# Kernel optimization log

Measured on AMD Instinct MI355X. Metric: run time of the kernel, lower is better.

Reference implementation:

```python
import jax, jax.numpy as jnp
import numpy as np

S, B, E, H = 2048, 2, 1024, 16
DH = E // H
SCALING = DH ** -0.5


def setup_inputs() -> dict:
    key = jax.random.key(0)
    ks = jax.random.split(key, 9)
    std = 1.0 / np.sqrt(E)
    return {
        "query": jax.random.normal(ks[0], (S, B, E), jnp.float32),
        "wq": jax.random.normal(ks[1], (E, E), jnp.float32) * std,
        "bq": jax.random.normal(ks[2], (E,), jnp.float32) * 0.02,
        "wk": jax.random.normal(ks[3], (E, E), jnp.float32) * std,
        "bk": jax.random.normal(ks[4], (E,), jnp.float32) * 0.02,
        "wv": jax.random.normal(ks[5], (E, E), jnp.float32) * std,
        "bv": jax.random.normal(ks[6], (E,), jnp.float32) * 0.02,
        "wo": jax.random.normal(ks[7], (E, E), jnp.float32) * std,
        "bo": jax.random.normal(ks[8], (E,), jnp.float32) * 0.02,
    }


def reference(query, wq, bq, wk, bk, wv, bv, wo, bo):
    # query: [S, B, E] (time, batch, channel), self-attention: key=value=query
    q = (query @ wq.T + bq) * SCALING          # fairseq scales q, not scores
    k = query @ wk.T + bk
    v = query @ wv.T + bv
    # split heads: [S, B, H, DH]
    q = q.reshape(S, B, H, DH)
    k = k.reshape(S, B, H, DH)
    v = v.reshape(S, B, H, DH)
    scores = jnp.einsum("qbhd,kbhd->bhqk", q, k)   # [B, H, S, S]
    probs = jax.nn.softmax(scores, axis=-1)
    ctx = jnp.einsum("bhqk,kbhd->qbhd", probs, v)  # [S, B, H, DH]
    ctx = ctx.reshape(S, B, E)
    return ctx @ wo.T + bo                          # [S, B, E]
```

## Files before the change

### kernel.cpp

```cpp
#include <hip/hip_runtime.h>
#include <hip/hip_bf16.h>
#include <stdint.h>

#define S_LEN 2048
#define BATCH 2
#define EMB   1024
#define NH    16
#define DHEAD 64
#define ROWS  (S_LEN*BATCH)
#define SCALE_Q 0.18033688011112042f
#define DEFER_THR 11.0f

typedef __attribute__((ext_vector_type(8))) short bf16x8;
typedef __attribute__((ext_vector_type(4))) float f32x4;
typedef __attribute__((ext_vector_type(16))) float f32x16;

typedef const __attribute__((address_space(1))) void* gas_ptr;
typedef __attribute__((address_space(3))) void* las_ptr;
#define GLD16(g, l) __builtin_amdgcn_global_load_lds((gas_ptr)(g), (las_ptr)(l), 16, 0, 0)

__device__ __forceinline__ unsigned short f2b(float f) {
  union { float f; unsigned int u; } v; v.f = f;
  unsigned int u = v.u;
  unsigned int r = (u + 0x7FFFu + ((u >> 16) & 1u)) >> 16;
  return (unsigned short)r;
}

__device__ __forceinline__ unsigned cvt_pk_bf16(float lo, float hi) {
  unsigned r;
  asm("v_cvt_pk_bf16_f32 %0, %1, %2" : "=v"(r) : "v"(lo), "v"(hi));
  return r;
}

__device__ __forceinline__ float exp2_raw(float x) {
  float r;
  asm("v_exp_f32 %0, %1" : "=v"(r) : "v"(x));
  return r;
}

__device__ __forceinline__ void cvt8(const float* __restrict__ s,
                                     unsigned short* __restrict__ d, size_t i) {
  float4 a = *reinterpret_cast<const float4*>(s + i);
  float4 b = *reinterpret_cast<const float4*>(s + i + 4);
  uint4 o;
  o.x = (unsigned)f2b(a.x) | ((unsigned)f2b(a.y) << 16);
  o.y = (unsigned)f2b(a.z) | ((unsigned)f2b(a.w) << 16);
  o.z = (unsigned)f2b(b.x) | ((unsigned)f2b(b.y) << 16);
  o.w = (unsigned)f2b(b.z) | ((unsigned)f2b(b.w) << 16);
  *reinterpret_cast<uint4*>(d + i) = o;
}

__global__ __launch_bounds__(256) void cvt_all_kernel(
    const float* __restrict__ query,
    const float* __restrict__ wq, const float* __restrict__ wk,
    const float* __restrict__ wv, const float* __restrict__ wo,
    unsigned short* __restrict__ Xbf,
    unsigned short* __restrict__ Wqb, unsigned short* __restrict__ Wkb,
    unsigned short* __restrict__ Wvb, unsigned short* __restrict__ Wob) {
  int id = blockIdx.x;
  const float* s; unsigned short* d; size_t off;
  if (id < 2048) { s = query; d = Xbf; off = (size_t)id * 2048; }
  else {
    int wsel = (id - 2048) >> 9;
    off = (size_t)((id - 2048) & 511) * 2048;
    switch (wsel) {
      case 0:  s = wq; d = Wqb; break;
      case 1:  s = wk; d = Wkb; break;
      case 2:  s = wv; d = Wvb; break;
      default: s = wo; d = Wob; break;
    }
  }
  cvt8(s, d, off + (size_t)threadIdx.x * 8);
}

__device__ __forceinline__ void gemm_mainloop(const unsigned short* __restrict__ A,
                                              const unsigned short* __restrict__ Bw,
                                              int m0, int n0, f32x4 acc[4][4],
                                              unsigned short* Ab, unsigned short* Bb) {
  const int t    = threadIdx.x;
  const int lane = t & 63;
  const int w    = t >> 6;
  const int wr   = w >> 1, wc = w & 1;
  const int lm   = lane & 15;
  const int lq   = lane >> 4;

  f32x4 zf = {0.0f, 0.0f, 0.0f, 0.0f};
#pragma unroll
  for (int i = 0; i < 4; ++i)
#pragma unroll
    for (int j = 0; j < 4; ++j) acc[i][j] = zf;

  for (int k0 = 0; k0 < EMB; k0 += 64) {
#pragma unroll
    for (int q = 0; q < 4; ++q) {
      int c = t + q * 256;
      int r = c >> 3, ci = c & 7;
      int lc = ci ^ (r & 7);
      GLD16(A  + (size_t)(m0 + r) * EMB + k0 + lc * 8,
            (char*)Ab + (size_t)(q * 256 + w * 64) * 16);
      GLD16(Bw + (size_t)(n0 + r) * EMB + k0 + lc * 8,
            (char*)Bb + (size_t)(q * 256 + w * 64) * 16);
    }
    asm volatile("s_waitcnt vmcnt(0)" ::: "memory");
    __syncthreads();

#pragma unroll
    for (int kk = 0; kk < 2; ++kk) {
      bf16x8 af[4], bfr[4];
#pragma unroll
      for (int i = 0; i < 4; ++i) {
        int ra = wr * 64 + i * 16 + lm;
        af[i] = *reinterpret_cast<const bf16x8*>(
            &Ab[ra * 64 + ((kk * 4 + lq) ^ (ra & 7)) * 8]);
      }
#pragma unroll
      for (int j = 0; j < 4; ++j) {
        int rb = wc * 64 + j * 16 + lm;
        bfr[j] = *reinterpret_cast<const bf16x8*>(
            &Bb[rb * 64 + ((kk * 4 + lq) ^ (rb & 7)) * 8]);
      }
#pragma unroll
      for (int i = 0; i < 4; ++i)
#pragma unroll
        for (int j = 0; j < 4; ++j)
          acc[i][j] = __builtin_amdgcn_mfma_f32_16x16x32_bf16(af[i], bfr[j], acc[i][j], 0, 0, 0);
    }
    __syncthreads();
  }
}

__global__ __launch_bounds__(256) void gemm_qkv_kernel(
    const unsigned short* __restrict__ X,
    const unsigned short* __restrict__ Wq, const unsigned short* __restrict__ Wk,
    const unsigned short* __restrict__ Wv,
    const float* __restrict__ bq, const float* __restrict__ bk, const float* __restrict__ bv,
    unsigned short* __restrict__ Qb, unsigned short* __restrict__ Kb,
    unsigned short* __restrict__ Vtg) {
  __shared__ unsigned short SH[2][128 * 64];
  const int m0 = blockIdx.x * 128;
  const int n0 = blockIdx.y * 128;
  const int z  = blockIdx.z;
  const unsigned short* Bw = (z == 0) ? Wq : (z == 1) ? Wk : Wv;
  const float* bias        = (z == 0) ? bq : (z == 1) ? bk : bv;

  f32x4 acc[4][4];
  gemm_mainloop(X, Bw, m0, n0, acc, SH[0], SH[1]);

  const int t    = threadIdx.x;
  const int lane = t & 63;
  const int w    = t >> 6;
  const int wr   = w >> 1, wc = w & 1;
  const int lm   = lane & 15, lq = lane >> 4;

  if (z != 2) {
    unsigned short* Out = (z == 0) ? Qb : Kb;
    const float scale   = (z == 0) ? SCALE_Q : 1.0f;
#pragma unroll
    for (int j = 0; j < 4; ++j) {
      int col = n0 + wc * 64 + j * 16 + lm;
      int h = col >> 6, dd = col & 63;
      float bc = bias[col];
#pragma unroll
      for (int i = 0; i < 4; ++i) {
#pragma unroll
        for (int r = 0; r < 4; ++r) {
          int row = m0 + wr * 64 + i * 16 + lq * 4 + r;
          int s = row >> 1, b = row & 1;
          float v = (acc[i][j][r] + bc) * scale;
          Out[((size_t)(b * NH + h) * S_LEN + s) * DHEAD + dd] = f2b(v);
        }
      }
    }
  } else {
    unsigned short* T = &SH[0][0];
#pragma unroll
    for (int j = 0; j < 4; ++j) {
      int col = wc * 64 + j * 16 + lm;
      float bc = bias[n0 + col];
#pragma unroll
      for (int i = 0; i < 4; ++i) {
#pragma unroll
        for (int r = 0; r < 4; ++r) {
          int row = wr * 64 + i * 16 + lq * 4 + r;
          int idx = (row & 1) * 64 + (row >> 1);
          int chunk = idx >> 3, within = idx & 7;
          int pchunk = (chunk & 8) | ((chunk ^ col) & 7);
          T[col * 128 + pchunk * 8 + within] = f2b(acc[i][j][r] + bc);
        }
      }
    }
    __syncthreads();
#pragma unroll
    for (int itr = 0; itr < 8; ++itr) {
      int u = (t >> 3) + itr * 32;
      int col = u & 127, b = u >> 7;
      int c3 = t & 7;
      int pchunk = (b * 8) | ((c3 ^ col) & 7);
      bf16x8 vv = *reinterpret_cast<const bf16x8*>(&T[col * 128 + pchunk * 8]);
      int h = (n0 + col) >> 6, dd = (n0 + col) & 63;
      unsigned short* dst =
          Vtg + ((size_t)(b * NH + h) * DHEAD + dd) * S_LEN + (m0 >> 1);
      int p1 = ((c3 >> 1) << 4) | ((c3 & 1) << 2);
      union { bf16x8 v; uint4 u4; } cv; cv.v = vv;
      *reinterpret_cast<uint2*>(dst + p1)     = make_uint2(cv.u4.x, cv.u4.y);
      *reinterpret_cast<uint2*>(dst + p1 + 8) = make_uint2(cv.u4.z, cv.u4.w);
    }
  }
}

__global__ __launch_bounds__(256) void gemm_out_kernel(
    const unsigned short* __restrict__ Ctx, const unsigned short* __restrict__ Wo,
    const float* __restrict__ bo, float* __restrict__ Out) {
  __shared__ unsigned short Ab[64 * 64];
  __shared__ unsigned short Bb[128 * 64];
  const int m0 = blockIdx.x * 64;
  const int n0 = blockIdx.y * 128;
  const int t    = threadIdx.x;
  const int lane = t & 63;
  const int w    = t >> 6;
  const int wr   = w >> 1, wc = w & 1;
  const int lm   = lane & 15, lq = lane >> 4;

  f32x4 zf = {0.0f, 0.0f, 0.0f, 0.0f};
  f32x4 acc[2][4];
#pragma unroll
  for (int i = 0; i < 2; ++i)
#pragma unroll
    for (int j = 0; j < 4; ++j) acc[i][j] = zf;

  for (int k0 = 0; k0 < EMB; k0 += 64) {
#pragma unroll
    for (int q = 0; q < 2; ++q) {
      int c = t + q * 256;
      int r = c >> 3, ci = c & 7;
      int lc = ci ^ (r & 7);
      GLD16(Ctx + (size_t)(m0 + r) * EMB + k0 + lc * 8,
            (char*)Ab + (size_t)(q * 256 + w * 64) * 16);
    }
#pragma unroll
    for (int q = 0; q < 4; ++q) {
      int c = t + q * 256;
      int r = c >> 3, ci = c & 7;
      int lc = ci ^ (r & 7);
      GLD16(Wo + (size_t)(n0 + r) * EMB + k0 + lc * 8,
            (char*)Bb + (size_t)(q * 256 + w * 64) * 16);
    }
    asm volatile("s_waitcnt vmcnt(0)" ::: "memory");
    __syncthreads();

#pragma unroll
    for (int kk = 0; kk < 2; ++kk) {
      bf16x8 af[2], bfr[4];
#pragma unroll
      for (int i = 0; i < 2; ++i) {
        int ra = wr * 32 + i * 16 + lm;
        af[i] = *reinterpret_cast<const bf16x8*>(
            &Ab[ra * 64 + ((kk * 4 + lq) ^ (ra & 7)) * 8]);
      }
#pragma unroll
      for (int j = 0; j < 4; ++j) {
        int rb = wc * 64 + j * 16 + lm;
        bfr[j] = *reinterpret_cast<const bf16x8*>(
            &Bb[rb * 64 + ((kk * 4 + lq) ^ (rb & 7)) * 8]);
      }
#pragma unroll
      for (int i = 0; i < 2; ++i)
#pragma unroll
        for (int j = 0; j < 4; ++j)
          acc[i][j] = __builtin_amdgcn_mfma_f32_16x16x32_bf16(af[i], bfr[j], acc[i][j], 0, 0, 0);
    }
    __syncthreads();
  }

#pragma unroll
  for (int j = 0; j < 4; ++j) {
    int col = n0 + wc * 64 + j * 16 + lm;
    float bc = bo[col];
#pragma unroll
    for (int i = 0; i < 2; ++i) {
#pragma unroll
      for (int r = 0; r < 4; ++r) {
        int row = m0 + wr * 32 + i * 16 + lq * 4 + r;
        Out[(size_t)row * EMB + col] = acc[i][j][r] + bc;
      }
    }
  }
}

__global__ __launch_bounds__(512, 4) void attn_kernel(
    const unsigned short* __restrict__ Qb, const unsigned short* __restrict__ Kb,
    const unsigned short* __restrict__ Vtg, unsigned short* __restrict__ Ctx) {
  const int bh = blockIdx.x;
  const int q0 = blockIdx.y * 128;
  const int t    = threadIdx.x;
  const int lane = t & 63;
  const int w    = t >> 6;
  const int hf   = w >> 2;
  const int wl   = w & 3;
  const int th   = t & 255;
  const int l31  = lane & 31;
  const int hh   = lane >> 5;
  const unsigned short* Q  = Qb  + (size_t)bh * S_LEN * DHEAD;
  const unsigned short* K  = Kb  + (size_t)bh * S_LEN * DHEAD;
  const unsigned short* Vt = Vtg + (size_t)bh * DHEAD * S_LEN;

  alignas(16) __shared__ char SMEM[65536];
  unsigned short* Kl = (unsigned short*)(SMEM + hf * 32768);
  unsigned short* Vl = (unsigned short*)(SMEM + hf * 32768 + 16384);

  const int qw = q0 + wl * 32;

  bf16x8 aq[4];
#pragma unroll
  for (int kk = 0; kk < 4; ++kk)
    aq[kk] = *reinterpret_cast<const bf16x8*>(
        Q + (size_t)(qw + l31) * DHEAD + kk * 16 + hh * 8);

  f32x16 z16 = {0.f,0.f,0.f,0.f, 0.f,0.f,0.f,0.f, 0.f,0.f,0.f,0.f, 0.f,0.f,0.f,0.f};
  f32x16 accO[2];
  accO[0] = z16; accO[1] = z16;
  float m_s = -1e30f, l_s = 0.0f;

  auto STAGE = [&](int b, int kb) {
#pragma unroll
    for (int q = 0; q < 2; ++q) {
      int c = th + q * 256;
      int r = c >> 3, pp = c & 7;
      int lc = pp ^ (r & 7);
      GLD16(K + (size_t)(kb + r) * DHEAD + lc * 8,
            (char*)Kl + (size_t)b * 8192 + (size_t)(q * 256 + wl * 64) * 16);
      GLD16(Vt + (size_t)r * S_LEN + kb + lc * 8,
            (char*)Vl + (size_t)b * 8192 + (size_t)(q * 256 + wl * 64) * 16);
    }
  };

  const int kvbase = hf * (S_LEN / 2);
  const int NT = S_LEN / 2 / 64;
  STAGE(0, kvbase);
  STAGE(1, kvbase + 64);

  for (int it = 0; it < NT; ++it) {
    const int cur = it & 1;
    if (it < NT - 1) {
      asm volatile("s_waitcnt vmcnt(4)" ::: "memory");
    } else {
      asm volatile("s_waitcnt vmcnt(0)" ::: "memory");
    }
    __builtin_amdgcn_s_barrier();

    const unsigned short* Klc = Kl + cur * 4096;
    const unsigned short* Vlc = Vl + cur * 4096;

    f32x16 p32[2];
    __builtin_amdgcn_s_setprio(1);
#pragma unroll
    for (int ji = 0; ji < 2; ++ji) {
      f32x16 a = z16;
      int rr = ji * 32 + l31;
#pragma unroll
      for (int kk = 0; kk < 4; ++kk) {
        bf16x8 kf = *reinterpret_cast<const bf16x8*>(
            &Klc[rr * 64 + ((kk * 2 + hh) ^ (rr & 7)) * 8]);
        a = __builtin_amdgcn_mfma_f32_32x32x16_bf16(kf, aq[kk], a, 0, 0, 0);
      }
      p32[ji] = a;
    }
    __builtin_amdgcn_s_setprio(0);

    float t8[8];
#pragma unroll
    for (int e = 0; e < 8; ++e)
      t8[e] = fmaxf(fmaxf(p32[0][e], p32[0][e + 8]),
                    fmaxf(p32[1][e], p32[1][e + 8]));
    float u0 = fmaxf(t8[0], t8[4]), u1 = fmaxf(t8[1], t8[5]);
    float u2 = fmaxf(t8[2], t8[6]), u3 = fmaxf(t8[3], t8[7]);
    float tm = fmaxf(fmaxf(u0, u1), fmaxf(u2, u3));
    tm = fmaxf(tm, __shfl_xor(tm, 32));

    if (!__all(tm - m_s <= DEFER_THR)) {
      float mn = fmaxf(m_s, tm);
      float sc = exp2_raw(m_s - mn);
      l_s *= sc;
      m_s = mn;
#pragma unroll
      for (int r = 0; r < 16; ++r) {
        float scr = __shfl(sc, (r & 3) + 8 * (r >> 2) + 4 * hh);
        accO[0][r] *= scr;
        accO[1][r] *= scr;
      }
    }

#pragma unroll
    for (int e = 0; e < 16; ++e) {
      p32[0][e] = exp2_raw(p32[0][e] - m_s);
      p32[1][e] = exp2_raw(p32[1][e] - m_s);
    }
    float s8[8];
#pragma unroll
    for (int e = 0; e < 8; ++e)
      s8[e] = (p32[0][e] + p32[0][e + 8]) + (p32[1][e] + p32[1][e + 8]);
    float v0 = (s8[0] + s8[4]) + (s8[1] + s8[5]);
    float v1 = (s8[2] + s8[6]) + (s8[3] + s8[7]);
    float ps = v0 + v1;
    ps += __shfl_xor(ps, 32);
    l_s += ps;

    bf16x8 pa[2][2];
#pragma unroll
    for (int ji = 0; ji < 2; ++ji) {
      uint4 lo4, hi4;
      lo4.x = cvt_pk_bf16(p32[ji][0],  p32[ji][1]);
      lo4.y = cvt_pk_bf16(p32[ji][2],  p32[ji][3]);
      lo4.z = cvt_pk_bf16(p32[ji][4],  p32[ji][5]);
      lo4.w = cvt_pk_bf16(p32[ji][6],  p32[ji][7]);
      hi4.x = cvt_pk_bf16(p32[ji][8],  p32[ji][9]);
      hi4.y = cvt_pk_bf16(p32[ji][10], p32[ji][11]);
      hi4.z = cvt_pk_bf16(p32[ji][12], p32[ji][13]);
      hi4.w = cvt_pk_bf16(p32[ji][14], p32[ji][15]);
      pa[ji][0] = *reinterpret_cast<bf16x8*>(&lo4);
      pa[ji][1] = *reinterpret_cast<bf16x8*>(&hi4);
    }

    __builtin_amdgcn_s_setprio(1);
#pragma unroll
    for (int ni = 0; ni < 2; ++ni) {
      int dd = ni * 32 + l31;
#pragma unroll
      for (int ji = 0; ji < 2; ++ji)
#pragma unroll
        for (int ss = 0; ss < 2; ++ss) {
          bf16x8 bv = *reinterpret_cast<const bf16x8*>(
              &Vlc[dd * 64 + ((ji * 4 + ss * 2 + hh) ^ (dd & 7)) * 8]);
          accO[ni] = __builtin_amdgcn_mfma_f32_32x32x16_bf16(pa[ji][ss], bv, accO[ni], 0, 0, 0);
        }
    }
    __builtin_amdgcn_s_setprio(0);

    asm volatile("s_waitcnt lgkmcnt(0)" ::: "memory");
    __builtin_amdgcn_sched_barrier(0);
    __builtin_amdgcn_s_barrier();

    if (it + 2 < NT) STAGE(cur, kvbase + (it + 2) * 64);
  }

  float* MB = (float*)SMEM;
  const int MS = 35;
  const int mb = (wl * 64 + lane) * MS;
  if (hf == 1) {
    MB[mb]     = m_s;
    MB[mb + 1] = l_s;
#pragma unroll
    for (int r = 0; r < 16; ++r) {
      MB[mb + 2 + r]  = accO[0][r];
      MB[mb + 18 + r] = accO[1][r];
    }
  }
  __syncthreads();
  if (hf == 0) {
    float m1 = MB[mb], l1 = MB[mb + 1];
    float mn  = fmaxf(m_s, m1);
    float sc0 = exp2_raw(m_s - mn);
    float sc1 = exp2_raw(m1 - mn);
    float lf  = l_s * sc0 + l1 * sc1;
    const int b = bh >> 4, h = bh & 15;
#pragma unroll
    for (int r = 0; r < 16; ++r) {
      int row = (r & 3) + 8 * (r >> 2) + 4 * hh;
      float s0 = __shfl(sc0, row);
      float s1 = __shfl(sc1, row);
      float rl = 1.0f / __shfl(lf, row);
      float o0 = (accO[0][r] * s0 + MB[mb + 2 + r]  * s1) * rl;
      float o1 = (accO[1][r] * s0 + MB[mb + 18 + r] * s1) * rl;
      int srow = qw + row;
      size_t base = ((size_t)srow * BATCH + b) * EMB + (size_t)h * 64 + l31;
      Ctx[base]      = f2b(o0);
      Ctx[base + 32] = f2b(o1);
    }
  }
}

extern "C" void kernel_launch(void* const* d_in, const int* in_sizes, int n_in,
                              void* d_out, int out_size, void* d_ws, size_t ws_size,
                              hipStream_t stream) {
  const float* query = (const float*)d_in[0];
  const float* wq = (const float*)d_in[1];
  const float* bq = (const float*)d_in[2];
  const float* wk = (const float*)d_in[3];
  const float* bk = (const float*)d_in[4];
  const float* wv = (const float*)d_in[5];
  const float* bv = (const float*)d_in[6];
  const float* wo = (const float*)d_in[7];
  const float* bo = (const float*)d_in[8];
  float* out = (float*)d_out;

  unsigned short* p = (unsigned short*)d_ws;
  unsigned short* Xbf = p;                        p += (size_t)ROWS * EMB;
  unsigned short* Wqb = p;                        p += (size_t)EMB * EMB;
  unsigned short* Wkb = p;                        p += (size_t)EMB * EMB;
  unsigned short* Wvb = p;                        p += (size_t)EMB * EMB;
  unsigned short* Wob = p;                        p += (size_t)EMB * EMB;
  unsigned short* Qb  = p;                        p += (size_t)ROWS * EMB;
  unsigned short* Kb  = p;                        p += (size_t)ROWS * EMB;
  unsigned short* Vtg = p;                        p += (size_t)ROWS * EMB;
  unsigned short* Ctx = p;                        p += (size_t)ROWS * EMB;

  cvt_all_kernel<<<4096, 256, 0, stream>>>(query, wq, wk, wv, wo,
                                           Xbf, Wqb, Wkb, Wvb, Wob);
  gemm_qkv_kernel<<<dim3(ROWS / 128, EMB / 128, 3), 256, 0, stream>>>(
      Xbf, Wqb, Wkb, Wvb, bq, bk, bv, Qb, Kb, Vtg);
  attn_kernel<<<dim3(BATCH * NH, S_LEN / 128), 512, 0, stream>>>(Qb, Kb, Vtg, Ctx);
  gemm_out_kernel<<<dim3(ROWS / 64, EMB / 128), 256, 0, stream>>>(Ctx, Wob, bo, out);
}
```

Baseline: 194.9 us.

## Triple-buffer GEMM mainloop with async prefetch and retile output projection

Replaces the single-buffered GEMM mainloop (load, wait, compute, sync each 64-wide k step) with a templated three-stage pipeline over 32-wide k tiles. Loads for tile it+2 are issued while tile it is computed, with partial vmcnt waits and raised wave priority around the MFMA block. The output projection now uses 128x128 tiles with 8 waves instead of 64x128 with 4 waves, and the V transpose epilogue gains a sync because the shared buffer is reused. The aim is to hide global-to-LDS latency in both projection GEMMs, at the cost of more LDS per block and more barriers per unit of k.

```diff
diff --git a/kernel.cpp b/kernel.cpp
--- a/kernel.cpp
+++ b/kernel.cpp
@@ -73,59 +73,81 @@
   cvt8(s, d, off + (size_t)threadIdx.x * 8);
 }
 
-__device__ __forceinline__ void gemm_mainloop(const unsigned short* __restrict__ A,
-                                              const unsigned short* __restrict__ Bw,
-                                              int m0, int n0, f32x4 acc[4][4],
-                                              unsigned short* Ab, unsigned short* Bb) {
+template <int NWAVE, int NJ>
+__device__ __forceinline__ void gemm_pipe(const unsigned short* __restrict__ A,
+                                          const unsigned short* __restrict__ Bw,
+                                          int m0, int n0, f32x4 (&acc)[4][NJ],
+                                          unsigned short* __restrict__ SH) {
+  const int T   = NWAVE * 64;
+  const int GQ  = 512 / T;
   const int t    = threadIdx.x;
   const int lane = t & 63;
   const int w    = t >> 6;
-  const int wr   = w >> 1, wc = w & 1;
-  const int lm   = lane & 15;
-  const int lq   = lane >> 4;
+  const int wcw  = NWAVE / 2;
+  const int wr   = w / wcw, wc = w % wcw;
+  const int nspan = 128 / wcw;
+  const int lm = lane & 15, lq = lane >> 4;
+  unsigned short* Ab = SH;
+  unsigned short* Bb = SH + 3 * 4096;
 
   f32x4 zf = {0.0f, 0.0f, 0.0f, 0.0f};
 #pragma unroll
   for (int i = 0; i < 4; ++i)
 #pragma unroll
-    for (int j = 0; j < 4; ++j) acc[i][j] = zf;
-
-  for (int k0 = 0; k0 < EMB; k0 += 64) {
-#pragma unroll
-    for (int q = 0; q < 4; ++q) {
-      int c = t + q * 256;
-      int r = c >> 3, ci = c & 7;
-      int lc = ci ^ (r & 7);
+    for (int j = 0; j < NJ; ++j) acc[i][j] = zf;
+
+  auto STAGE = [&](int buf, int k0) {
+#pragma unroll
+    for (int q = 0; q < GQ; ++q) {
+      int c = t + q * T;
+      int r = c >> 2, ci = c & 3;
+      int lc = ci ^ (r & 3);
       GLD16(A  + (size_t)(m0 + r) * EMB + k0 + lc * 8,
-            (char*)Ab + (size_t)(q * 256 + w * 64) * 16);
+            (char*)Ab + buf * 8192 + (size_t)(q * T + w * 64) * 16);
       GLD16(Bw + (size_t)(n0 + r) * EMB + k0 + lc * 8,
-            (char*)Bb + (size_t)(q * 256 + w * 64) * 16);
-    }
-    asm volatile("s_waitcnt vmcnt(0)" ::: "memory");
-    __syncthreads();
-
-#pragma unroll
-    for (int kk = 0; kk < 2; ++kk) {
-      bf16x8 af[4], bfr[4];
-#pragma unroll
-      for (int i = 0; i < 4; ++i) {
-        int ra = wr * 64 + i * 16 + lm;
-        af[i] = *reinterpret_cast<const bf16x8*>(
-            &Ab[ra * 64 + ((kk * 4 + lq) ^ (ra & 7)) * 8]);
-      }
-#pragma unroll
-      for (int j = 0; j < 4; ++j) {
-        int rb = wc * 64 + j * 16 + lm;
-        bfr[j] = *reinterpret_cast<const bf16x8*>(
-            &Bb[rb * 64 + ((kk * 4 + lq) ^ (rb & 7)) * 8]);
-      }
-#pragma unroll
-      for (int i = 0; i < 4; ++i)
-#pragma unroll
-        for (int j = 0; j < 4; ++j)
-          acc[i][j] = __builtin_amdgcn_mfma_f32_16x16x32_bf16(af[i], bfr[j], acc[i][j], 0, 0, 0);
-    }
-    __syncthreads();
+            (char*)Bb + buf * 8192 + (size_t)(q * T + w * 64) * 16);
+    }
+  };
+
+  const int NT = EMB / 32;
+  STAGE(0, 0);
+  STAGE(1, 32);
+  if (GQ == 2) { asm volatile("s_waitcnt vmcnt(4)" ::: "memory"); }
+  else         { asm volatile("s_waitcnt vmcnt(2)" ::: "memory"); }
+  __builtin_amdgcn_s_barrier();
+
+  for (int it = 0; it < NT; ++it) {
+    const int cur = it % 3;
+    const unsigned short* Ac = Ab + cur * 4096;
+    const unsigned short* Bc = Bb + cur * 4096;
+    bf16x8 af[4], bfr[NJ];
+#pragma unroll
+    for (int i = 0; i < 4; ++i) {
+      int ra = wr * 64 + i * 16 + lm;
+      af[i] = *reinterpret_cast<const bf16x8*>(&Ac[ra * 32 + (lq ^ (ra & 3)) * 8]);
+    }
+#pragma unroll
+    for (int j = 0; j < NJ; ++j) {
+      int rb = wc * nspan + j * 16 + lm;
+      bfr[j] = *reinterpret_cast<const bf16x8*>(&Bc[rb * 32 + (lq ^ (rb & 3)) * 8]);
+    }
+    __builtin_amdgcn_s_setprio(1);
+#pragma unroll
+    for (int i = 0; i < 4; ++i)
+#pragma unroll
+      for (int j = 0; j < NJ; ++j)
+        acc[i][j] = __builtin_amdgcn_mfma_f32_16x16x32_bf16(af[i], bfr[j], acc[i][j], 0, 0, 0);
+    __builtin_amdgcn_s_setprio(0);
+
+    if (it + 2 < NT) {
+      STAGE((it + 2) % 3, (it + 2) * 32);
+      if (GQ == 2) asm volatile("s_waitcnt vmcnt(4) lgkmcnt(0)" ::: "memory");
+      else         asm volatile("s_waitcnt vmcnt(2) lgkmcnt(0)" ::: "memory");
+    } else {
+      asm volatile("s_waitcnt vmcnt(0) lgkmcnt(0)" ::: "memory");
+    }
+    __builtin_amdgcn_sched_barrier(0);
+    __builtin_amdgcn_s_barrier();
   }
 }
 
@@ -136,7 +158,7 @@
     const float* __restrict__ bq, const float* __restrict__ bk, const float* __restrict__ bv,
     unsigned short* __restrict__ Qb, unsigned short* __restrict__ Kb,
     unsigned short* __restrict__ Vtg) {
-  __shared__ unsigned short SH[2][128 * 64];
+  __shared__ unsigned short SH[24576];
   const int m0 = blockIdx.x * 128;
   const int n0 = blockIdx.y * 128;
   const int z  = blockIdx.z;
@@ -144,7 +166,7 @@
   const float* bias        = (z == 0) ? bq : (z == 1) ? bk : bv;
 
   f32x4 acc[4][4];
-  gemm_mainloop(X, Bw, m0, n0, acc, SH[0], SH[1]);
+  gemm_pipe<4, 4>(X, Bw, m0, n0, acc, SH);
 
   const int t    = threadIdx.x;
   const int lane = t & 63;
@@ -172,7 +194,8 @@
       }
     }
   } else {
-    unsigned short* T = &SH[0][0];
+    unsigned short* T = SH;
+    __syncthreads();
 #pragma unroll
     for (int j = 0; j < 4; ++j) {
       int col = wc * 64 + j * 16 + lm;
@@ -208,79 +231,30 @@
   }
 }
 
-__global__ __launch_bounds__(256) void gemm_out_kernel(
+__global__ __launch_bounds__(512) void gemm_out_kernel(
     const unsigned short* __restrict__ Ctx, const unsigned short* __restrict__ Wo,
     const float* __restrict__ bo, float* __restrict__ Out) {
-  __shared__ unsigned short Ab[64 * 64];
-  __shared__ unsigned short Bb[128 * 64];
-  const int m0 = blockIdx.x * 64;
+  __shared__ unsigned short SH[24576];
+  const int m0 = blockIdx.x * 128;
   const int n0 = blockIdx.y * 128;
+
+  f32x4 acc[4][2];
+  gemm_pipe<8, 2>(Ctx, Wo, m0, n0, acc, SH);
+
   const int t    = threadIdx.x;
   const int lane = t & 63;
   const int w    = t >> 6;
-  const int wr   = w >> 1, wc = w & 1;
+  const int wr   = w >> 2, wc = w & 3;
   const int lm   = lane & 15, lq = lane >> 4;
-
-  f32x4 zf = {0.0f, 0.0f, 0.0f, 0.0f};
-  f32x4 acc[2][4];
-#pragma unroll
-  for (int i = 0; i < 2; ++i)
-#pragma unroll
-    for (int j = 0; j < 4; ++j) acc[i][j] = zf;
-
-  for (int k0 = 0; k0 < EMB; k0 += 64) {
-#pragma unroll
-    for (int q = 0; q < 2; ++q) {
-      int c = t + q * 256;
-      int r = c >> 3, ci = c & 7;
-      int lc = ci ^ (r & 7);
-      GLD16(Ctx + (size_t)(m0 + r) * EMB + k0 + lc * 8,
-            (char*)Ab + (size_t)(q * 256 + w * 64) * 16);
-    }
-#pragma unroll
-    for (int q = 0; q < 4; ++q) {
-      int c = t + q * 256;
-      int r = c >> 3, ci = c & 7;
-      int lc = ci ^ (r & 7);
-      GLD16(Wo + (size_t)(n0 + r) * EMB + k0 + lc * 8,
-            (char*)Bb + (size_t)(q * 256 + w * 64) * 16);
-    }
-    asm volatile("s_waitcnt vmcnt(0)" ::: "memory");
-    __syncthreads();
-
-#pragma unroll
-    for (int kk = 0; kk < 2; ++kk) {
-      bf16x8 af[2], bfr[4];
-#pragma unroll
-      for (int i = 0; i < 2; ++i) {
-        int ra = wr * 32 + i * 16 + lm;
-        af[i] = *reinterpret_cast<const bf16x8*>(
-            &Ab[ra * 64 + ((kk * 4 + lq) ^ (ra & 7)) * 8]);
-      }
-#pragma unroll
-      for (int j = 0; j < 4; ++j) {
-        int rb = wc * 64 + j * 16 + lm;
-        bfr[j] = *reinterpret_cast<const bf16x8*>(
-            &Bb[rb * 64 + ((kk * 4 + lq) ^ (rb & 7)) * 8]);
-      }
-#pragma unroll
-      for (int i = 0; i < 2; ++i)
-#pragma unroll
-        for (int j = 0; j < 4; ++j)
-          acc[i][j] = __builtin_amdgcn_mfma_f32_16x16x32_bf16(af[i], bfr[j], acc[i][j], 0, 0, 0);
-    }
-    __syncthreads();
-  }
-
-#pragma unroll
-  for (int j = 0; j < 4; ++j) {
-    int col = n0 + wc * 64 + j * 16 + lm;
+#pragma unroll
+  for (int j = 0; j < 2; ++j) {
+    int col = n0 + wc * 32 + j * 16 + lm;
     float bc = bo[col];
 #pragma unroll
-    for (int i = 0; i < 2; ++i) {
+    for (int i = 0; i < 4; ++i) {
 #pragma unroll
       for (int r = 0; r < 4; ++r) {
-        int row = m0 + wr * 32 + i * 16 + lq * 4 + r;
+        int row = m0 + wr * 64 + i * 16 + lq * 4 + r;
         Out[(size_t)row * EMB + col] = acc[i][j][r] + bc;
       }
     }
@@ -509,5 +483,5 @@
   gemm_qkv_kernel<<<dim3(ROWS / 128, EMB / 128, 3), 256, 0, stream>>>(
       Xbf, Wqb, Wkb, Wvb, bq, bk, bv, Qb, Kb, Vtg);
   attn_kernel<<<dim3(BATCH * NH, S_LEN / 128), 512, 0, stream>>>(Qb, Kb, Vtg, Ctx);
-  gemm_out_kernel<<<dim3(ROWS / 64, EMB / 128), 256, 0, stream>>>(Ctx, Wob, bo, out);
-}
+  gemm_out_kernel<<<dim3(ROWS / 128, EMB / 128), 512, 0, stream>>>(Ctx, Wob, bo, out);
+}
```

New measurement: 194.6 us. About the same (-0.2%).
